# Performance work log

Measured on AMD Instinct MI355X. Metric: run time of the kernel, lower is better.

The kernel has to match this reference:

```python
import jax, jax.numpy as jnp
import numpy as np

# static config (matches init_kwargs / input_specs)
B, S, D, H, DH = 4, 2048, 2048, 16, 128
MAX_LEN = 1024  # round_up_to_multiple_of_256(max ragged length); lengths below max at 1024
ROPE_BASE = 10000.0


def setup_inputs() -> dict:
    key = jax.random.key(0)
    ks = jax.random.split(key, 8)
    q_src = jax.random.normal(ks[0], (B, MAX_LEN, D), jnp.float32)
    k_src = jax.random.normal(ks[1], (B, S, D), jnp.float32)
    v_src = jax.random.normal(ks[2], (B, S, D), jnp.float32)
    std = 1.0 / np.sqrt(D)
    Wq = jax.random.normal(ks[3], (D, H * DH), jnp.float32) * std
    Wk = jax.random.normal(ks[4], (D, H * DH), jnp.float32) * std
    Wv = jax.random.normal(ks[5], (D, H * DH), jnp.float32) * std
    Wo = jax.random.normal(ks[6], (H * DH, D), jnp.float32) * (1.0 / np.sqrt(H * DH))
    # mask[0]: causal bool [B,S,S]; mask[1]: full position ids [B,S]
    mask0 = jnp.broadcast_to(jnp.tril(jnp.ones((S, S), bool)), (B, S, S))
    pos_full = jnp.broadcast_to(jnp.arange(S, dtype=jnp.int32), (B, S))
    # ragged skip_mask: row i keeps lengths[i] random positions (max 1024 -> MAX_LEN)
    lengths = jnp.array([1024, 896, 768, 640], jnp.int32)
    scores = jax.random.uniform(ks[7], (B, S))
    ranks = jnp.argsort(jnp.argsort(scores, axis=1), axis=1)
    skip_mask = ranks < lengths[:, None]
    return {"q_src": q_src, "k_src": k_src, "v_src": v_src,
            "Wq": Wq, "Wk": Wk, "Wv": Wv, "Wo": Wo,
            "mask0": mask0, "pos_full": pos_full, "skip_mask": skip_mask}


def _rope(x, positions):
    # x: [B,H,L,DH], positions: [B,L] int -> rotary embedding on full head dim
    dh = x.shape[-1]
    inv_freq = 1.0 / (ROPE_BASE ** (jnp.arange(0, dh, 2, dtype=jnp.float32) / dh))
    freqs = positions.astype(jnp.float32)[:, :, None] * inv_freq      # [B,L,dh/2]
    emb = jnp.concatenate([freqs, freqs], axis=-1)[:, None]           # [B,1,L,dh]
    x1, x2 = jnp.split(x, 2, axis=-1)
    rot = jnp.concatenate([-x2, x1], axis=-1)                         # rotate_half
    return x * jnp.cos(emb) + rot * jnp.sin(emb)


def reference(q_src, k_src, v_src, Wq, Wk, Wv, Wo, mask0, pos_full, skip_mask):
    def heads(x, W):
        y = x @ W
        return y.reshape(x.shape[0], x.shape[1], H, DH).transpose(0, 2, 1, 3)

    q = heads(q_src, Wq)   # [B,H,MAX_LEN,DH]
    k = heads(k_src, Wk)   # [B,H,S,DH]
    v = heads(v_src, Wv)   # [B,H,S,DH]

    # _trim_attention_mask: gather kept rows (True-first, stable order), pad to MAX_LEN
    order = jnp.argsort(jnp.where(skip_mask, 0, 1), axis=1)[:, :MAX_LEN]  # [B,MAX_LEN]
    n = skip_mask.sum(axis=1)                                             # ragged lengths
    valid = jnp.arange(MAX_LEN)[None, :] < n[:, None]                     # [B,MAX_LEN]
    amask = jnp.take_along_axis(mask0, order[:, :, None], axis=1) & valid[:, :, None]
    pos_trim = jnp.where(valid, jnp.take_along_axis(pos_full, order, axis=1), 0)

    # RoPE: trimmed positions for q, full positions for k
    q = _rope(q, pos_trim)
    k = _rope(k, pos_full)

    # masked SDPA; fully-masked (padded) query rows -> zero output
    logits = jnp.einsum('bhld,bhsd->bhls', q, k) / np.sqrt(DH).astype(np.float32)
    logits = jnp.where(amask[:, None], logits, jnp.finfo(logits.dtype).min)
    probs = jax.nn.softmax(logits, axis=-1) * valid[:, None, :, None]
    ctx = jnp.einsum('bhls,bhsd->bhld', probs, v)                         # [B,H,MAX_LEN,DH]

    out = ctx.transpose(0, 2, 1, 3).reshape(B, MAX_LEN, H * DH) @ Wo     # [B,MAX_LEN,D]
    return out
```

## Files before the change

kernel.cpp:

```cpp
#include <hip/hip_runtime.h>

#define BB 4
#define SS 2048
#define DD 2048
#define HH 16
#define DHD 128
#define MAXL 1024

typedef __bf16 bf16x8 __attribute__((ext_vector_type(8)));
typedef float f32x4 __attribute__((ext_vector_type(4)));
typedef unsigned int u32_as1 __attribute__((address_space(1)));
typedef unsigned int u32_as3 __attribute__((address_space(3)));

__device__ __forceinline__ unsigned short f2bf(float f) {
  unsigned int u = __builtin_bit_cast(unsigned int, f);
  u += 0x7fffu + ((u >> 16) & 1u);
  return (unsigned short)(u >> 16);
}
__device__ __forceinline__ float bf2f(unsigned short h) {
  unsigned int u = ((unsigned int)h) << 16;
  return __builtin_bit_cast(float, u);
}
union U4 { uint4 u; bf16x8 b; };
__device__ __forceinline__ bf16x8 ldfrag(const unsigned short* p) {
  U4 x; x.u = *(const uint4*)p; return x.b;
}
__device__ __forceinline__ void gl_lds16(const void* g, void* l) {
  __builtin_amdgcn_global_load_lds((const u32_as1*)g, (u32_as3*)l, 16, 0, 0);
}

__global__ void build_pos(const int* __restrict__ skip, int* __restrict__ posk,
                          int* __restrict__ nval) {
  int b = blockIdx.x, t = threadIdx.x;
  __shared__ int cnts[64], offs[64];
  const int* row = skip + b * SS;
  int c = 0;
  for (int i = 0; i < 32; i++) c += (row[t * 32 + i] != 0);
  cnts[t] = c;
  __syncthreads();
  if (t == 0) {
    int run = 0;
    for (int i = 0; i < 64; i++) { offs[i] = run; run += cnts[i]; }
    nval[b] = run > MAXL ? MAXL : run;
  }
  __syncthreads();
  int o = offs[t];
  for (int i = 0; i < 32; i++)
    if (row[t * 32 + i]) { if (o < MAXL) posk[b * MAXL + o] = t * 32 + i; o++; }
  int nb = nval[b];
  for (int l = nb + t; l < MAXL; l += 64) posk[b * MAXL + l] = -1;
}

__global__ __launch_bounds__(256) void cvt3(const float* __restrict__ q,
                                            const float* __restrict__ k,
                                            const float* __restrict__ v,
                                            unsigned short* __restrict__ oq,
                                            unsigned short* __restrict__ ok,
                                            unsigned short* __restrict__ ov) {
  const int nq = BB * MAXL * DD / 4, nk = BB * SS * DD / 4;
  int idx = blockIdx.x * 256 + threadIdx.x;
  const float* src; unsigned short* dst; int off;
  if (idx < nq) { src = q; dst = oq; off = idx; }
  else if (idx < nq + nk) { src = k; dst = ok; off = idx - nq; }
  else { src = v; dst = ov; off = idx - nq - nk; }
  float4 vv = ((const float4*)src)[off];
  ushort4 h;
  h.x = f2bf(vv.x); h.y = f2bf(vv.y); h.z = f2bf(vv.z); h.w = f2bf(vv.w);
  ((ushort4*)dst)[off] = h;
}

__global__ __launch_bounds__(256) void transpose_w4(const float* __restrict__ w0,
    const float* __restrict__ w1, const float* __restrict__ w2, const float* __restrict__ w3,
    unsigned short* __restrict__ o0, unsigned short* __restrict__ o1,
    unsigned short* __restrict__ o2, unsigned short* __restrict__ o3) {
  __shared__ __align__(16) unsigned short tile[64 * 76];
  const float* W; unsigned short* Wt;
  switch (blockIdx.z) {
    case 0: W = w0; Wt = o0; break;
    case 1: W = w1; Wt = o1; break;
    case 2: W = w2; Wt = o2; break;
    default: W = w3; Wt = o3; break;
  }
  int tx = threadIdx.x;
  int K0 = blockIdx.y * 64, N0 = blockIdx.x * 64;
  #pragma unroll
  for (int i = 0; i < 4; i++) {
    int r = (tx >> 4) + i * 16, c4 = (tx & 15) * 4;
    float4 v = *(const float4*)&W[(size_t)(K0 + r) * DD + N0 + c4];
    ushort4 h;
    h.x = f2bf(v.x); h.y = f2bf(v.y); h.z = f2bf(v.z); h.w = f2bf(v.w);
    *(ushort4*)&tile[r * 76 + c4] = h;
  }
  __syncthreads();
  #pragma unroll
  for (int i = 0; i < 4; i++) {
    int n = (tx >> 4) + i * 16, k4 = (tx & 15) * 4;
    ushort4 h;
    h.x = tile[(k4 + 0) * 76 + n];
    h.y = tile[(k4 + 1) * 76 + n];
    h.z = tile[(k4 + 2) * 76 + n];
    h.w = tile[(k4 + 3) * 76 + n];
    *(ushort4*)&Wt[(size_t)(N0 + n) * DD + K0 + k4] = h;
  }
}

__global__ __launch_bounds__(256) void gemm_bt(const unsigned short* __restrict__ A,
                                               const unsigned short* __restrict__ Bt,
                                               void* __restrict__ Cp,
                                               int M, int N, int K, int mode, int Lbits) {
  __shared__ __align__(16) unsigned short buf[4 * 4352];
  unsigned short* As = buf;
  unsigned short* Bs = buf + 4096;
  const int tid = threadIdx.x;
  const int lane = tid & 63, quad = lane >> 4, c = lane & 15;
  const int w = tid >> 6;
  const int wm = (w >> 1) * 64, wn = (w & 1) * 64;
  const size_t tm = (size_t)blockIdx.y * 128, tn = (size_t)blockIdx.x * 128;

  f32x4 acc[4][4] = {};

  const int srow = tid >> 2, scol = (tid & 3) * 8;
  const unsigned short* ga = A + (tm + srow) * K + scol;
  const unsigned short* gb = Bt + (tn + srow) * K + scol;
  unsigned short* la = &As[tid * 8];
  unsigned short* lb = &Bs[tid * 8];

  for (int kk = 0; kk < K; kk += 32) {
    gl_lds16(ga + kk, la);
    gl_lds16(ga + kk + (size_t)64 * K, la + 2048);
    gl_lds16(gb + kk, lb);
    gl_lds16(gb + kk + (size_t)64 * K, lb + 2048);
    __syncthreads();
    bf16x8 af[4], bfr[4];
    #pragma unroll
    for (int i = 0; i < 4; i++) af[i] = ldfrag(&As[(wm + i * 16 + c) * 32 + quad * 8]);
    #pragma unroll
    for (int j = 0; j < 4; j++) bfr[j] = ldfrag(&Bs[(wn + j * 16 + c) * 32 + quad * 8]);
    #pragma unroll
    for (int i = 0; i < 4; i++)
      #pragma unroll
      for (int j = 0; j < 4; j++)
        acc[i][j] = __builtin_amdgcn_mfma_f32_16x16x32_bf16(af[i], bfr[j], acc[i][j], 0, 0, 0);
    __syncthreads();
  }

  if (mode == 1) {
    float* Cf = (float*)Cp;
    #pragma unroll
    for (int i = 0; i < 4; i++)
      #pragma unroll
      for (int j = 0; j < 4; j++)
        #pragma unroll
        for (int r = 0; r < 4; r++) {
          size_t m = tm + wm + i * 16 + quad * 4 + r;
          size_t n = tn + wn + j * 16 + c;
          Cf[m * N + n] = acc[i][j][r];
        }
    return;
  }
  unsigned short* Cb = (unsigned short*)Cp;
  unsigned short* ep = buf + w * 4352;
  if (mode == 0) {
    #pragma unroll
    for (int i = 0; i < 4; i++)
      #pragma unroll
      for (int j = 0; j < 4; j++)
        #pragma unroll
        for (int r = 0; r < 4; r++)
          ep[(i * 16 + quad * 4 + r) * 68 + j * 16 + c] = f2bf(acc[i][j][r]);
    const size_t Lmask = ((size_t)1 << Lbits) - 1;
    #pragma unroll
    for (int it = 0; it < 8; it++) {
      int chunk = it * 64 + lane;
      int ml = chunk >> 3, nc = (chunk & 7) * 8;
      uint4 val = *(const uint4*)&ep[ml * 68 + nc];
      size_t m = tm + wm + ml, n = tn + wn + nc;
      size_t b = m >> Lbits, l = m & Lmask, h = n >> 7, d = n & 127;
      *(uint4*)&Cb[(((b * HH + h) << Lbits) + l) * 128 + d] = val;
    }
  } else {
    #pragma unroll
    for (int i = 0; i < 4; i++)
      #pragma unroll
      for (int j = 0; j < 4; j++)
        #pragma unroll
        for (int r = 0; r < 4; r++)
          ep[(j * 16 + c) * 68 + i * 16 + quad * 4 + r] = f2bf(acc[i][j][r]);
    #pragma unroll
    for (int it = 0; it < 8; it++) {
      int chunk = it * 64 + lane;
      int nl = chunk >> 3, mc = (chunk & 7) * 8;
      uint4 val = *(const uint4*)&ep[nl * 68 + mc];
      size_t n = tn + wn + nl, m = tm + wm + mc;
      size_t b = m >> 11, s = m & 2047, h = n >> 7, d = n & 127;
      *(uint4*)&Cb[((b * HH + h) * 128 + d) * SS + s] = val;
    }
  }
}

__global__ __launch_bounds__(256) void rope2(unsigned short* __restrict__ xq,
                                             unsigned short* __restrict__ xk,
                                             const int* __restrict__ posk) {
  const int Nq = BB * HH * MAXL * 64;
  int gid = blockIdx.x * 256 + threadIdx.x;
  unsigned short* x; int Lbits, idx, use_posk;
  if (gid < Nq) { x = xq; Lbits = 10; use_posk = 1; idx = gid; }
  else { x = xk; Lbits = 11; use_posk = 0; idx = gid - Nq; }
  int d = idx & 63;
  int rest = idx >> 6;
  int l = rest & ((1 << Lbits) - 1);
  int bh = rest >> Lbits;
  int b = bh >> 4;
  int p = use_posk ? posk[(b << 10) + l] : l;
  float ang = (float)p * __expf(-(float)d * 0.14391156831212787f);
  float sn, cs;
  __sincosf(ang, &sn, &cs);
  size_t base = (size_t)rest * 128;
  float x1 = bf2f(x[base + d]), x2 = bf2f(x[base + d + 64]);
  x[base + d]      = f2bf(x1 * cs - x2 * sn);
  x[base + d + 64] = f2bf(x2 * cs + x1 * sn);
}

__global__ __launch_bounds__(256) void attn_kernel(const unsigned short* __restrict__ qp,
                                                   const unsigned short* __restrict__ kp,
                                                   const unsigned short* __restrict__ vtp,
                                                   const int* __restrict__ posk,
                                                   const int* __restrict__ nval,
                                                   unsigned short* __restrict__ ctx) {
  __shared__ __align__(16) unsigned short k_s[64 * 128];
  __shared__ __align__(16) unsigned short vt_s[128 * 64];
  __shared__ __align__(16) unsigned short p_s[4 * 16 * 72];
  __shared__ int km_s[64];

  const int tid = threadIdx.x;
  const int w = tid >> 6, lane = tid & 63, quad = lane >> 4, c = lane & 15;
  const int bh = blockIdx.x, b = bh >> 4, h = bh & 15;
  const int qbase = blockIdx.y * 64;
  const int nb = nval[b];

  if (tid < 64) {
    int l = qbase + tid;
    km_s[tid] = (l < nb) ? posk[(b << 10) + l] : -1;
  }
  __syncthreads();

  const unsigned short* qg = qp + (((size_t)bh << 10) + qbase) * 128;
  bf16x8 aq[4];
  #pragma unroll
  for (int ks = 0; ks < 4; ks++)
    aq[ks] = ldfrag(&qg[(size_t)(w * 16 + c) * 128 + ks * 32 + quad * 8]);

  int lv = nb - 1 - qbase; lv = lv > 63 ? 63 : lv;
  const int tile_kmax = (lv >= 0) ? km_s[lv] : -1;
  const int nkt = (tile_kmax >= 0) ? ((tile_kmax >> 6) + 1) : 0;

  int km[4];
  #pragma unroll
  for (int r = 0; r < 4; r++) km[r] = km_s[w * 16 + quad * 4 + r];

  const int srow = tid >> 4;
  const int kswz = (tid & 15) ^ (srow & 7);
  const unsigned short* kgp = kp + ((size_t)bh << 11) * 128 + (size_t)srow * 128 + kswz * 8;
  const int dvrow = tid >> 3;
  const int vswz = (tid & 7) ^ (dvrow & 7);
  const unsigned short* vgp = vtp + ((size_t)bh * 128 + dvrow) * SS + vswz * 8;

  float m_i[4], l_i[4];
  #pragma unroll
  for (int r = 0; r < 4; r++) { m_i[r] = -1e30f; l_i[r] = 0.f; }
  f32x4 o[8];
  #pragma unroll
  for (int dj = 0; dj < 8; dj++) o[dj] = (f32x4){0.f, 0.f, 0.f, 0.f};

  for (int kt = 0; kt < nkt; kt++) {
    const int kb = kt * 64;
    __syncthreads();
    #pragma unroll
    for (int i = 0; i < 4; i++)
      gl_lds16(kgp + ((size_t)kb + i * 16) * 128, &k_s[(i * 256 + tid) * 8]);
    #pragma unroll
    for (int i = 0; i < 4; i++)
      gl_lds16(vgp + (size_t)kb + (size_t)i * 32 * SS, &vt_s[(i * 256 + tid) * 8]);
    __syncthreads();

    f32x4 sa[4];
    #pragma unroll
    for (int j = 0; j < 4; j++) {
      sa[j] = (f32x4){0.f, 0.f, 0.f, 0.f};
      #pragma unroll
      for (int ks = 0; ks < 4; ks++) {
        bf16x8 bk = ldfrag(&k_s[((j * 16 + c) << 7) + (((ks * 4 + quad) ^ (c & 7)) << 3)]);
        sa[j] = __builtin_amdgcn_mfma_f32_16x16x32_bf16(aq[ks], bk, sa[j], 0, 0, 0);
      }
    }

    const float scale = 0.08838834764831843f;
    float mt[4] = {-1e30f, -1e30f, -1e30f, -1e30f};
    #pragma unroll
    for (int j = 0; j < 4; j++) {
      int key = kb + j * 16 + c;
      #pragma unroll
      for (int r = 0; r < 4; r++) {
        float v = (key <= km[r]) ? sa[j][r] * scale : -1e30f;
        sa[j][r] = v;
        mt[r] = fmaxf(mt[r], v);
      }
    }
    #pragma unroll
    for (int r = 0; r < 4; r++)
      for (int off = 1; off < 16; off <<= 1)
        mt[r] = fmaxf(mt[r], __shfl_xor(mt[r], off, 16));
    float al[4], rs[4];
    #pragma unroll
    for (int r = 0; r < 4; r++) {
      float mn = fmaxf(m_i[r], mt[r]);
      al[r] = __expf(m_i[r] - mn);
      m_i[r] = mn;
      rs[r] = 0.f;
    }
    #pragma unroll
    for (int j = 0; j < 4; j++)
      #pragma unroll
      for (int r = 0; r < 4; r++) {
        float pv = __expf(sa[j][r] - m_i[r]);
        sa[j][r] = pv;
        rs[r] += pv;
      }
    #pragma unroll
    for (int r = 0; r < 4; r++) {
      for (int off = 1; off < 16; off <<= 1) rs[r] += __shfl_xor(rs[r], off, 16);
      l_i[r] = l_i[r] * al[r] + rs[r];
    }
    #pragma unroll
    for (int dj = 0; dj < 8; dj++)
      #pragma unroll
      for (int r = 0; r < 4; r++) o[dj][r] *= al[r];

    #pragma unroll
    for (int j = 0; j < 4; j++)
      #pragma unroll
      for (int r = 0; r < 4; r++)
        p_s[w * 1152 + (quad * 4 + r) * 72 + j * 16 + c] = f2bf(sa[j][r]);

    #pragma unroll
    for (int ks2 = 0; ks2 < 2; ks2++) {
      bf16x8 ap = ldfrag(&p_s[w * 1152 + c * 72 + ks2 * 32 + quad * 8]);
      #pragma unroll
      for (int dj = 0; dj < 8; dj++) {
        bf16x8 bv = ldfrag(&vt_s[((dj * 16 + c) << 6) + (((ks2 * 4 + quad) ^ (c & 7)) << 3)]);
        o[dj] = __builtin_amdgcn_mfma_f32_16x16x32_bf16(ap, bv, o[dj], 0, 0, 0);
      }
    }
  }

  #pragma unroll
  for (int r = 0; r < 4; r++) {
    int l = qbase + w * 16 + quad * 4 + r;
    bool ok = (l < nb);
    float inv = ok ? (1.0f / l_i[r]) : 0.0f;
    #pragma unroll
    for (int dj = 0; dj < 8; dj++)
      ctx[(((size_t)b << 10) + l) * (size_t)DD + h * 128 + dj * 16 + c] =
          f2bf(ok ? o[dj][r] * inv : 0.0f);
  }
}

extern "C" void kernel_launch(void* const* d_in, const int* in_sizes, int n_in,
                              void* d_out, int out_size, void* d_ws, size_t ws_size,
                              hipStream_t stream) {
  const float* q_src = (const float*)d_in[0];
  const float* k_src = (const float*)d_in[1];
  const float* v_src = (const float*)d_in[2];
  const float* Wq = (const float*)d_in[3];
  const float* Wk = (const float*)d_in[4];
  const float* Wv = (const float*)d_in[5];
  const float* Wo = (const float*)d_in[6];
  const int* skip = (const int*)d_in[9];

  char* p = (char*)d_ws;
  auto alloc = [&](size_t bytes) -> char* {
    char* r = p;
    p += (bytes + 255) & ~(size_t)255;
    return r;
  };
  unsigned short* a_q  = (unsigned short*)alloc((size_t)BB * MAXL * DD * 2);
  unsigned short* a_k  = (unsigned short*)alloc((size_t)BB * SS * DD * 2);
  unsigned short* a_v  = (unsigned short*)alloc((size_t)BB * SS * DD * 2);
  unsigned short* wt_q = (unsigned short*)alloc((size_t)DD * DD * 2);
  unsigned short* wt_k = (unsigned short*)alloc((size_t)DD * DD * 2);
  unsigned short* wt_v = (unsigned short*)alloc((size_t)DD * DD * 2);
  unsigned short* wt_o = (unsigned short*)alloc((size_t)DD * DD * 2);
  unsigned short* q_pro = (unsigned short*)alloc((size_t)BB * HH * MAXL * DHD * 2);
  unsigned short* k_pro = (unsigned short*)alloc((size_t)BB * HH * SS * DHD * 2);
  unsigned short* v_t   = (unsigned short*)alloc((size_t)BB * HH * SS * DHD * 2);
  int* posk = (int*)alloc((size_t)BB * MAXL * 4);
  int* nval = (int*)alloc(64);
  unsigned short* ctx = a_q;

  build_pos<<<BB, 64, 0, stream>>>(skip, posk, nval);
  cvt3<<<(BB * MAXL * DD + 2 * BB * SS * DD) / (4 * 256), 256, 0, stream>>>(
      q_src, k_src, v_src, a_q, a_k, a_v);
  transpose_w4<<<dim3(32, 32, 4), 256, 0, stream>>>(Wq, Wk, Wv, Wo, wt_q, wt_k, wt_v, wt_o);

  gemm_bt<<<dim3(16, 32), 256, 0, stream>>>(a_q, wt_q, q_pro, BB * MAXL, DD, DD, 0, 10);
  gemm_bt<<<dim3(16, 64), 256, 0, stream>>>(a_k, wt_k, k_pro, BB * SS, DD, DD, 0, 11);
  gemm_bt<<<dim3(16, 64), 256, 0, stream>>>(a_v, wt_v, v_t, BB * SS, DD, DD, 2, 11);

  rope2<<<(BB * HH * (MAXL + SS) * 64) / 256, 256, 0, stream>>>(q_pro, k_pro, posk);

  attn_kernel<<<dim3(BB * HH, MAXL / 64), 256, 0, stream>>>(q_pro, k_pro, v_t, posk, nval, ctx);

  gemm_bt<<<dim3(16, 32), 256, 0, stream>>>(ctx, wt_o, d_out, BB * MAXL, DD, DD, 1, 0);
}
```

Measured before the change: 759.6 us.

## Replace 128x128 GEMM with double-buffered swizzled 256x256 tile kernel

Replaces the projection/output GEMM with a 512-thread kernel computing 256x256 tiles with a K step of 64. It double-buffers global-to-LDS loads with explicit vmcnt waits, XOR-swizzles the LDS layout to avoid bank conflicts, and interleaves fragment loads with MFMA groups using barriers and setprio. Blocks are remapped across XCDs for cache locality. The intent is higher MFMA utilization and more operand reuse. In exchange it uses 128KB of LDS per block, and the Q and output GEMMs launch only 128 blocks, which may leave many CUs idle.

New measurement: 763.0 us. No clear change (+0.5%).

```diff
diff --git a/kernel.cpp b/kernel.cpp
--- a/kernel.cpp
+++ b/kernel.cpp
@@ -104,50 +104,129 @@
   }
 }
 
-__global__ __launch_bounds__(256) void gemm_bt(const unsigned short* __restrict__ A,
-                                               const unsigned short* __restrict__ Bt,
-                                               void* __restrict__ Cp,
-                                               int M, int N, int K, int mode, int Lbits) {
-  __shared__ __align__(16) unsigned short buf[4 * 4352];
-  unsigned short* As = buf;
-  unsigned short* Bs = buf + 4096;
+__global__ __launch_bounds__(512, 2) void gemm256(const unsigned short* __restrict__ A,
+                                                  const unsigned short* __restrict__ Bt,
+                                                  void* __restrict__ Cp,
+                                                  int M, int N, int K, int mode, int Lbits) {
+  __shared__ __align__(16) unsigned short lds[65536];
+
   const int tid = threadIdx.x;
   const int lane = tid & 63, quad = lane >> 4, c = lane & 15;
   const int w = tid >> 6;
-  const int wm = (w >> 1) * 64, wn = (w & 1) * 64;
-  const size_t tm = (size_t)blockIdx.y * 128, tn = (size_t)blockIdx.x * 128;
-
-  f32x4 acc[4][4] = {};
-
-  const int srow = tid >> 2, scol = (tid & 3) * 8;
-  const unsigned short* ga = A + (tm + srow) * K + scol;
-  const unsigned short* gb = Bt + (tn + srow) * K + scol;
-  unsigned short* la = &As[tid * 8];
-  unsigned short* lb = &Bs[tid * 8];
-
-  for (int kk = 0; kk < K; kk += 32) {
-    gl_lds16(ga + kk, la);
-    gl_lds16(ga + kk + (size_t)64 * K, la + 2048);
-    gl_lds16(gb + kk, lb);
-    gl_lds16(gb + kk + (size_t)64 * K, lb + 2048);
-    __syncthreads();
-    bf16x8 af[4], bfr[4];
-    #pragma unroll
-    for (int i = 0; i < 4; i++) af[i] = ldfrag(&As[(wm + i * 16 + c) * 32 + quad * 8]);
-    #pragma unroll
-    for (int j = 0; j < 4; j++) bfr[j] = ldfrag(&Bs[(wn + j * 16 + c) * 32 + quad * 8]);
-    #pragma unroll
-    for (int i = 0; i < 4; i++)
-      #pragma unroll
-      for (int j = 0; j < 4; j++)
-        acc[i][j] = __builtin_amdgcn_mfma_f32_16x16x32_bf16(af[i], bfr[j], acc[i][j], 0, 0, 0);
-    __syncthreads();
+  const int wm = (w >> 2) * 128, wn = (w & 3) * 64;
+
+  const int nwg = gridDim.x * gridDim.y;
+  const int bid0 = blockIdx.y * gridDim.x + blockIdx.x;
+  const int cpx = nwg >> 3;
+  const int bid = (bid0 & 7) * cpx + (bid0 >> 3);
+  const int bx = bid % gridDim.x;
+  const int by = bid / gridDim.x;
+  const size_t tm = (size_t)by * 256, tn = (size_t)bx * 256;
+
+  f32x4 acc[8][4] = {};
+
+  const int trow = tid >> 3;
+  const int tch = ((tid & 7) ^ (trow & 7)) * 8;
+  const unsigned short* gA = A + (tm + trow) * (size_t)K + tch;
+  const unsigned short* gB = Bt + (tn + trow) * (size_t)K + tch;
+
+  auto STAGE = [&](unsigned short* asd, unsigned short* bsd, int kk) {
+    #pragma unroll
+    for (int i = 0; i < 4; i++) {
+      gl_lds16(gA + kk + (size_t)(i * 64) * K, asd + i * 4096 + tid * 8);
+      gl_lds16(gB + kk + (size_t)(i * 64) * K, bsd + i * 4096 + tid * 8);
+    }
+  };
+
+  const int nkt = K >> 6;
+  STAGE(lds, lds + 32768, 0);
+
+  for (int t = 0; t < nkt; ++t) {
+    const int sel = t & 1;
+    const unsigned short* as = lds + sel * 16384;
+    const unsigned short* bs = lds + 32768 + sel * 16384;
+    if (t + 1 < nkt) {
+      const int s2 = sel ^ 1;
+      STAGE(lds + s2 * 16384, lds + 32768 + s2 * 16384, (t + 1) << 6);
+      asm volatile("s_waitcnt vmcnt(8)" ::: "memory");
+    } else {
+      asm volatile("s_waitcnt vmcnt(0)" ::: "memory");
+    }
+    __builtin_amdgcn_s_barrier();
+
+    bf16x8 af[4][2], ag[4][2], bfr[4][2];
+    #pragma unroll
+    for (int i = 0; i < 4; i++)
+      #pragma unroll
+      for (int ks = 0; ks < 2; ks++)
+        af[i][ks] = ldfrag(&as[(wm + i * 16 + c) * 64 + (((ks * 4 + quad) ^ (c & 7)) << 3)]);
+    #pragma unroll
+    for (int j = 0; j < 2; j++)
+      #pragma unroll
+      for (int ks = 0; ks < 2; ks++)
+        bfr[j][ks] = ldfrag(&bs[(wn + j * 16 + c) * 64 + (((ks * 4 + quad) ^ (c & 7)) << 3)]);
+    __builtin_amdgcn_s_barrier();
+    asm volatile("s_waitcnt lgkmcnt(0)" ::: "memory");
+    __builtin_amdgcn_s_setprio(1);
+    #pragma unroll
+    for (int i = 0; i < 4; i++)
+      #pragma unroll
+      for (int j = 0; j < 2; j++)
+        #pragma unroll
+        for (int ks = 0; ks < 2; ks++)
+          acc[i][j] = __builtin_amdgcn_mfma_f32_16x16x32_bf16(af[i][ks], bfr[j][ks], acc[i][j], 0, 0, 0);
+    __builtin_amdgcn_s_setprio(0);
+    __builtin_amdgcn_s_barrier();
+    #pragma unroll
+    for (int j = 2; j < 4; j++)
+      #pragma unroll
+      for (int ks = 0; ks < 2; ks++)
+        bfr[j][ks] = ldfrag(&bs[(wn + j * 16 + c) * 64 + (((ks * 4 + quad) ^ (c & 7)) << 3)]);
+    __builtin_amdgcn_s_barrier();
+    asm volatile("s_waitcnt lgkmcnt(0)" ::: "memory");
+    __builtin_amdgcn_s_setprio(1);
+    #pragma unroll
+    for (int i = 0; i < 4; i++)
+      #pragma unroll
+      for (int j = 2; j < 4; j++)
+        #pragma unroll
+        for (int ks = 0; ks < 2; ks++)
+          acc[i][j] = __builtin_amdgcn_mfma_f32_16x16x32_bf16(af[i][ks], bfr[j][ks], acc[i][j], 0, 0, 0);
+    __builtin_amdgcn_s_setprio(0);
+    __builtin_amdgcn_s_barrier();
+    #pragma unroll
+    for (int i = 0; i < 4; i++)
+      #pragma unroll
+      for (int ks = 0; ks < 2; ks++)
+        ag[i][ks] = ldfrag(&as[(wm + 64 + i * 16 + c) * 64 + (((ks * 4 + quad) ^ (c & 7)) << 3)]);
+    __builtin_amdgcn_s_barrier();
+    asm volatile("s_waitcnt lgkmcnt(0)" ::: "memory");
+    __builtin_amdgcn_s_setprio(1);
+    #pragma unroll
+    for (int i = 0; i < 4; i++)
+      #pragma unroll
+      for (int j = 0; j < 2; j++)
+        #pragma unroll
+        for (int ks = 0; ks < 2; ks++)
+          acc[4 + i][j] = __builtin_amdgcn_mfma_f32_16x16x32_bf16(ag[i][ks], bfr[j][ks], acc[4 + i][j], 0, 0, 0);
+    __builtin_amdgcn_s_setprio(0);
+    __builtin_amdgcn_s_barrier();
+    __builtin_amdgcn_s_setprio(1);
+    #pragma unroll
+    for (int i = 0; i < 4; i++)
+      #pragma unroll
+      for (int j = 2; j < 4; j++)
+        #pragma unroll
+        for (int ks = 0; ks < 2; ks++)
+          acc[4 + i][j] = __builtin_amdgcn_mfma_f32_16x16x32_bf16(ag[i][ks], bfr[j][ks], acc[4 + i][j], 0, 0, 0);
+    __builtin_amdgcn_s_setprio(0);
+    __builtin_amdgcn_s_barrier();
   }
 
   if (mode == 1) {
     float* Cf = (float*)Cp;
     #pragma unroll
-    for (int i = 0; i < 4; i++)
+    for (int i = 0; i < 8; i++)
       #pragma unroll
       for (int j = 0; j < 4; j++)
         #pragma unroll
@@ -159,41 +238,47 @@
     return;
   }
   unsigned short* Cb = (unsigned short*)Cp;
-  unsigned short* ep = buf + w * 4352;
+  unsigned short* ep = lds + w * 8192;
   if (mode == 0) {
-    #pragma unroll
-    for (int i = 0; i < 4; i++)
-      #pragma unroll
-      for (int j = 0; j < 4; j++)
-        #pragma unroll
-        for (int r = 0; r < 4; r++)
-          ep[(i * 16 + quad * 4 + r) * 68 + j * 16 + c] = f2bf(acc[i][j][r]);
     const size_t Lmask = ((size_t)1 << Lbits) - 1;
     #pragma unroll
-    for (int it = 0; it < 8; it++) {
-      int chunk = it * 64 + lane;
-      int ml = chunk >> 3, nc = (chunk & 7) * 8;
-      uint4 val = *(const uint4*)&ep[ml * 68 + nc];
-      size_t m = tm + wm + ml, n = tn + wn + nc;
-      size_t b = m >> Lbits, l = m & Lmask, h = n >> 7, d = n & 127;
-      *(uint4*)&Cb[(((b * HH + h) << Lbits) + l) * 128 + d] = val;
+    for (int mh = 0; mh < 2; mh++) {
+      #pragma unroll
+      for (int i = 0; i < 4; i++)
+        #pragma unroll
+        for (int j = 0; j < 4; j++)
+          #pragma unroll
+          for (int r = 0; r < 4; r++)
+            ep[(i * 16 + quad * 4 + r) * 68 + j * 16 + c] = f2bf(acc[mh * 4 + i][j][r]);
+      #pragma unroll
+      for (int it = 0; it < 8; it++) {
+        int chunk = it * 64 + lane;
+        int ml = chunk >> 3, nc = (chunk & 7) * 8;
+        uint4 val = *(const uint4*)&ep[ml * 68 + nc];
+        size_t m = tm + wm + mh * 64 + ml, n = tn + wn + nc;
+        size_t b = m >> Lbits, l = m & Lmask, h = n >> 7, d = n & 127;
+        *(uint4*)&Cb[(((b * HH + h) << Lbits) + l) * 128 + d] = val;
+      }
     }
   } else {
     #pragma unroll
-    for (int i = 0; i < 4; i++)
-      #pragma unroll
-      for (int j = 0; j < 4; j++)
-        #pragma unroll
-        for (int r = 0; r < 4; r++)
-          ep[(j * 16 + c) * 68 + i * 16 + quad * 4 + r] = f2bf(acc[i][j][r]);
-    #pragma unroll
-    for (int it = 0; it < 8; it++) {
-      int chunk = it * 64 + lane;
-      int nl = chunk >> 3, mc = (chunk & 7) * 8;
-      uint4 val = *(const uint4*)&ep[nl * 68 + mc];
-      size_t n = tn + wn + nl, m = tm + wm + mc;
-      size_t b = m >> 11, s = m & 2047, h = n >> 7, d = n & 127;
-      *(uint4*)&Cb[((b * HH + h) * 128 + d) * SS + s] = val;
+    for (int mh = 0; mh < 2; mh++) {
+      #pragma unroll
+      for (int i = 0; i < 4; i++)
+        #pragma unroll
+        for (int j = 0; j < 4; j++)
+          #pragma unroll
+          for (int r = 0; r < 4; r++)
+            ep[(j * 16 + c) * 68 + i * 16 + quad * 4 + r] = f2bf(acc[mh * 4 + i][j][r]);
+      #pragma unroll
+      for (int it = 0; it < 8; it++) {
+        int chunk = it * 64 + lane;
+        int nl = chunk >> 3, mc = (chunk & 7) * 8;
+        uint4 val = *(const uint4*)&ep[nl * 68 + mc];
+        size_t n = tn + wn + nl, m = tm + wm + mh * 64 + mc;
+        size_t b = m >> 11, s = m & 2047, h = n >> 7, d = n & 127;
+        *(uint4*)&Cb[((b * HH + h) * 128 + d) * SS + s] = val;
+      }
     }
   }
 }
@@ -402,13 +487,13 @@
       q_src, k_src, v_src, a_q, a_k, a_v);
   transpose_w4<<<dim3(32, 32, 4), 256, 0, stream>>>(Wq, Wk, Wv, Wo, wt_q, wt_k, wt_v, wt_o);
 
-  gemm_bt<<<dim3(16, 32), 256, 0, stream>>>(a_q, wt_q, q_pro, BB * MAXL, DD, DD, 0, 10);
-  gemm_bt<<<dim3(16, 64), 256, 0, stream>>>(a_k, wt_k, k_pro, BB * SS, DD, DD, 0, 11);
-  gemm_bt<<<dim3(16, 64), 256, 0, stream>>>(a_v, wt_v, v_t, BB * SS, DD, DD, 2, 11);
+  gemm256<<<dim3(8, 16), 512, 0, stream>>>(a_q, wt_q, q_pro, BB * MAXL, DD, DD, 0, 10);
+  gemm256<<<dim3(8, 32), 512, 0, stream>>>(a_k, wt_k, k_pro, BB * SS, DD, DD, 0, 11);
+  gemm256<<<dim3(8, 32), 512, 0, stream>>>(a_v, wt_v, v_t, BB * SS, DD, DD, 2, 11);
 
   rope2<<<(BB * HH * (MAXL + SS) * 64) / 256, 256, 0, stream>>>(q_pro, k_pro, posk);
 
   attn_kernel<<<dim3(BB * HH, MAXL / 64), 256, 0, stream>>>(q_pro, k_pro, v_t, posk, nval, ctx);
 
-  gemm_bt<<<dim3(16, 32), 256, 0, stream>>>(ctx, wt_o, d_out, BB * MAXL, DD, DD, 1, 0);
-}
+  gemm256<<<dim3(8, 16), 512, 0, stream>>>(ctx, wt_o, d_out, BB * MAXL, DD, DD, 1, 0);
+}
```
